# Kernel tuning notes

Measured on AMD Instinct MI355X. Metric: run time of the kernel, lower is better.

Reference implementation:

```python
import jax, jax.numpy as jnp
import numpy as np

N_NODES = 20000
N_EDGES = 640000
B = 256
GNN_DIM = 256
HID = 512
INNER = 2048
RANK = 512
N_CLASSES = 3
N_GENES = 6640


def _ln(x, s, b, eps=1e-5):
    mu = jnp.mean(x, axis=-1, keepdims=True)
    var = jnp.mean(jnp.square(x - mu), axis=-1, keepdims=True)
    return (x - mu) * jax.lax.rsqrt(var + eps) * s + b


def setup_inputs() -> dict:
    key = jax.random.key(0)
    ks = jax.random.split(key, 16)
    s = 0.02
    return {
        "node_indices": jax.random.randint(ks[0], (B,), 0, N_NODES, dtype=jnp.int32),
        "edge_index": jax.random.randint(ks[1], (2, N_EDGES), 0, N_NODES, dtype=jnp.int32),
        "edge_weight": jax.random.uniform(ks[2], (N_EDGES,), dtype=jnp.float32),
        "partial_emb": jax.random.normal(ks[3], (N_NODES, GNN_DIM), dtype=jnp.float32),
        "oov_emb": jnp.zeros((1, GNN_DIM), jnp.float32),
        "gnn_ln_s": jnp.ones((3, GNN_DIM), jnp.float32),
        "gnn_ln_b": jnp.zeros((3, GNN_DIM), jnp.float32),
        "gnn_w": jax.random.normal(ks[4], (3, GNN_DIM, GNN_DIM), jnp.float32) * s,
        "gnn_b": jnp.zeros((3, GNN_DIM), jnp.float32),
        "post_w": jax.random.normal(ks[5], (GNN_DIM, GNN_DIM), jnp.float32) * s,
        "post_b": jnp.zeros((GNN_DIM,), jnp.float32),
        "pin_w": jax.random.normal(ks[6], (GNN_DIM, HID), jnp.float32) * s,
        "pin_b": jnp.zeros((HID,), jnp.float32),
        "blk_ln_s": jnp.ones((6, HID), jnp.float32),
        "blk_ln_b": jnp.zeros((6, HID), jnp.float32),
        "blk_w1": jax.random.normal(ks[7], (6, HID, INNER), jnp.float32) * s,
        "blk_b1": jnp.zeros((6, INNER), jnp.float32),
        "blk_w2": jax.random.normal(ks[8], (6, INNER, HID), jnp.float32) * s,
        "blk_b2": jnp.zeros((6, HID), jnp.float32),
        "pout_w": jax.random.normal(ks[9], (HID, N_CLASSES * RANK), jnp.float32) * s,
        "pout_b": jnp.zeros((N_CLASSES * RANK,), jnp.float32),
        "out_gene_emb": jax.random.normal(ks[10], (N_GENES, RANK), jnp.float32) * s,
    }


def reference(node_indices, edge_index, edge_weight, partial_emb, oov_emb,
              gnn_ln_s, gnn_ln_b, gnn_w, gnn_b, post_w, post_b,
              pin_w, pin_b, blk_ln_s, blk_ln_b, blk_w1, blk_b1, blk_w2, blk_b2,
              pout_w, pout_b, out_gene_emb):
    n = partial_emb.shape[0]
    src, dst = edge_index[0], edge_index[1]
    # --- trainable GNN tail: 3 layers of (LN -> weighted scatter-sum -> Linear -> ReLU) + residual ---
    x = partial_emb
    for i in range(3):
        h = _ln(x, gnn_ln_s[i], gnn_ln_b[i])
        msg = h[src] * edge_weight[:, None]              # [E, 256] gather (memory-bound)
        agg = jax.ops.segment_sum(msg, dst, num_segments=n)
        h = jax.nn.relu(agg @ gnn_w[i] + gnn_b[i])
        x = h + x
    x = x @ post_w + post_b                              # post_mp
    # --- OOV-safe perturbation embedding lookup ---
    oov = node_indices < 0
    safe = jnp.where(oov, 0, node_indices)
    pert = jnp.where(oov[:, None], oov_emb, x[safe])     # [B, 256]
    # --- bilinear head ---
    h = pert @ pin_w + pin_b
    for i in range(6):
        z = _ln(h, blk_ln_s[i], blk_ln_b[i])
        z = jax.nn.gelu(z @ blk_w1[i] + blk_b1[i], approximate=False)
        h = h + z @ blk_w2[i] + blk_b2[i]                # dropout = identity (eval)
    proj = (h @ pout_w + pout_b).reshape(h.shape[0], N_CLASSES, RANK)
    logits = jnp.einsum('bcr,gr->bcg', proj, out_gene_emb)
    return logits
```

## Files before the change

### kernel.cpp

```cpp
#include <hip/hip_runtime.h>
#include <hip/hip_bf16.h>
#include <math.h>

#define NNODES 20000
#define NEDGES 640000
#define BSZ 256
#define GDIM 256
#define HID 512
#define INNER 2048
#define RANK 512
#define NCLS 3
#define NGENES 6640

typedef __attribute__((ext_vector_type(8))) short bf16x8;
typedef __attribute__((ext_vector_type(4))) float f32x4;
typedef __attribute__((ext_vector_type(4))) unsigned u32x4;

__device__ inline float bf2f(unsigned short u) {
    return __uint_as_float(((unsigned)u) << 16);
}
__device__ inline unsigned short f2bf(float f) {
    unsigned u = __float_as_uint(f);
    u = u + 0x7fff + ((u >> 16) & 1);
    return (unsigned short)(u >> 16);
}
__device__ inline unsigned pk2(float a, float b) {
    return (unsigned)f2bf(a) | ((unsigned)f2bf(b) << 16);
}

__device__ inline u32x4 ld16_cg(const void* p) {
    u32x4 r;
    asm volatile("global_load_dwordx4 %0, %1, off sc0 sc1" : "=v"(r) : "v"(p) : "memory");
    return r;
}
__device__ inline void st4f_cg(void* p, float v) {
    asm volatile("global_store_dword %0, %1, off sc0 sc1" :: "v"(p), "v"(v) : "memory");
}
__device__ inline void st2_cg(void* p, unsigned short v) {
    unsigned w = v;
    asm volatile("global_store_short %0, %1, off sc0 sc1" :: "v"(p), "v"(w) : "memory");
}
__device__ inline void waitvm0(void) {
    asm volatile("s_waitcnt vmcnt(0)" ::: "memory");
    __builtin_amdgcn_sched_barrier(0);
}

__global__ void hist_k(const int* __restrict__ dst, int* __restrict__ counts, int E) {
    int e = blockIdx.x * 256 + threadIdx.x;
    if (e < E) atomicAdd(&counts[dst[e]], 1);
}

__global__ void scan1_k(const int* __restrict__ counts, int* __restrict__ incl,
                        int* __restrict__ bsums, int n) {
    __shared__ int s[256];
    int i = blockIdx.x * 256 + threadIdx.x;
    int v = (i < n) ? counts[i] : 0;
    s[threadIdx.x] = v;
    __syncthreads();
    for (int off = 1; off < 256; off <<= 1) {
        int t = (threadIdx.x >= off) ? s[threadIdx.x - off] : 0;
        __syncthreads();
        s[threadIdx.x] += t;
        __syncthreads();
    }
    if (i < n) incl[i] = s[threadIdx.x];
    if (threadIdx.x == 255) bsums[blockIdx.x] = s[255];
}

__global__ void scan2_k(const int* __restrict__ bsums, int* __restrict__ boffs, int nb) {
    __shared__ int s[128];
    int tid = threadIdx.x;
    int v = (tid < nb) ? bsums[tid] : 0;
    s[tid] = v;
    __syncthreads();
    for (int off = 1; off < 128; off <<= 1) {
        int t = (tid >= off) ? s[tid - off] : 0;
        __syncthreads();
        s[tid] += t;
        __syncthreads();
    }
    if (tid < nb) boffs[tid] = s[tid] - v;
}

__global__ void scan3_k(const int* __restrict__ incl, const int* __restrict__ counts,
                        const int* __restrict__ boffs, int* __restrict__ row_start,
                        int* __restrict__ cursor, int n) {
    int i = blockIdx.x * 256 + threadIdx.x;
    if (i < n) {
        int st = incl[i] - counts[i] + boffs[blockIdx.x];
        row_start[i] = st;
        cursor[i] = st;
    }
}

__global__ void scatter_k(const int* __restrict__ src, const int* __restrict__ dst,
                          const float* __restrict__ w, int* __restrict__ cursor,
                          int2* __restrict__ ep, int E) {
    int e = blockIdx.x * 256 + threadIdx.x;
    if (e < E) {
        int d = dst[e];
        int p = atomicAdd(&cursor[d], 1);
        ep[p] = make_int2(src[e], __float_as_int(w[e]));
    }
}

__global__ void convall_k(const float* __restrict__ gnn_w, const float* __restrict__ post_w,
                          const float* __restrict__ pin_w, const float* __restrict__ blk_w1,
                          const float* __restrict__ blk_w2, const float* __restrict__ pout_w,
                          const float* __restrict__ gene, unsigned short* __restrict__ gnnT,
                          unsigned short* __restrict__ postT, unsigned short* __restrict__ pinT,
                          unsigned short* __restrict__ w1T, unsigned short* __restrict__ w2T,
                          unsigned short* __restrict__ poutT,
                          unsigned short* __restrict__ geneb) {
    int b = blockIdx.x;
    if (b >= 13440) {
        int t = b - 13440;
        const float4* xp = (const float4*)gene;
        int i = t * 512 + threadIdx.x * 2;
        float4 a = xp[i], c = xp[i + 1];
        *(ushort4*)(geneb + (size_t)i * 4) =
            make_ushort4(f2bf(a.x), f2bf(a.y), f2bf(a.z), f2bf(a.w));
        *(ushort4*)(geneb + (size_t)i * 4 + 4) =
            make_ushort4(f2bf(c.x), f2bf(c.y), f2bf(c.z), f2bf(c.w));
        return;
    }
    const float* W;
    unsigned short* WT;
    int K, N, tile;
    if (b < 192) {
        int l = b >> 6;
        tile = b & 63;
        W = gnn_w + (size_t)l * GDIM * GDIM;
        WT = gnnT + (size_t)l * GDIM * GDIM;
        K = GDIM; N = GDIM;
    } else if (b < 256) {
        tile = b - 192; W = post_w; WT = postT; K = GDIM; N = GDIM;
    } else if (b < 384) {
        tile = b - 256; W = pin_w; WT = pinT; K = GDIM; N = HID;
    } else if (b < 6528) {
        int t = b - 384;
        int l = t >> 10;
        tile = t & 1023;
        W = blk_w1 + (size_t)l * HID * INNER;
        WT = w1T + (size_t)l * INNER * HID;
        K = HID; N = INNER;
    } else if (b < 12672) {
        int t = b - 6528;
        int l = t >> 10;
        tile = t & 1023;
        W = blk_w2 + (size_t)l * INNER * HID;
        WT = w2T + (size_t)l * HID * INNER;
        K = INNER; N = HID;
    } else {
        tile = b - 12672; W = pout_w; WT = poutT; K = HID; N = NCLS * RANK;
    }
    __shared__ float s[32][33];
    int ntx = N >> 5;
    int k0 = (tile / ntx) << 5;
    int n0 = (tile % ntx) << 5;
    int tx = threadIdx.x & 31, ty = threadIdx.x >> 5;
#pragma unroll
    for (int i = 0; i < 4; i++)
        s[ty + 8 * i][tx] = W[(size_t)(k0 + ty + 8 * i) * N + n0 + tx];
    __syncthreads();
#pragma unroll
    for (int i = 0; i < 4; i++)
        WT[(size_t)(n0 + ty + 8 * i) * K + k0 + tx] = f2bf(s[tx][ty + 8 * i]);
}

__global__ void lnb_k(const float* __restrict__ X, const float* __restrict__ sc,
                      const float* __restrict__ bi, unsigned short* __restrict__ Y, int M) {
    int row = blockIdx.x * 4 + (threadIdx.x >> 6);
    int lane = threadIdx.x & 63;
    if (row >= M) return;
    float4 v = ((const float4*)(X + (size_t)row * GDIM))[lane];
    float sum = v.x + v.y + v.z + v.w;
#pragma unroll
    for (int off = 32; off >= 1; off >>= 1) sum += __shfl_xor(sum, off);
    float mu = sum / GDIM;
    float a = v.x - mu, b = v.y - mu, c = v.z - mu, d = v.w - mu;
    float sq = a * a + b * b + c * c + d * d;
#pragma unroll
    for (int off = 32; off >= 1; off >>= 1) sq += __shfl_xor(sq, off);
    float rstd = rsqrtf(sq / GDIM + 1e-5f);
    float4 s4 = ((const float4*)sc)[lane];
    float4 b4 = ((const float4*)bi)[lane];
    *(ushort4*)(Y + (size_t)row * GDIM + lane * 4) =
        make_ushort4(f2bf(a * rstd * s4.x + b4.x), f2bf(b * rstd * s4.y + b4.y),
                     f2bf(c * rstd * s4.z + b4.z), f2bf(d * rstd * s4.w + b4.w));
}

__device__ inline void agg_row(int beg, int cnt, int lane, const int2* __restrict__ ep,
                               const unsigned short* __restrict__ H, float& a0, float& a1,
                               float& a2, float& a3) {
    int t = 0;
    for (; t + 16 <= cnt; t += 16) {
        int2 e[16];
#pragma unroll
        for (int u = 0; u < 16; u++) e[u] = ep[beg + t + u];
        ushort4 v[16];
#pragma unroll
        for (int u = 0; u < 16; u++)
            v[u] = *(const ushort4*)(H + (size_t)e[u].x * GDIM + lane * 4);
#pragma unroll
        for (int u = 0; u < 16; u++) {
            float w = __int_as_float(e[u].y);
            a0 = fmaf(bf2f(v[u].x), w, a0);
            a1 = fmaf(bf2f(v[u].y), w, a1);
            a2 = fmaf(bf2f(v[u].z), w, a2);
            a3 = fmaf(bf2f(v[u].w), w, a3);
        }
    }
    for (; t + 4 <= cnt; t += 4) {
        int2 e[4];
#pragma unroll
        for (int u = 0; u < 4; u++) e[u] = ep[beg + t + u];
        ushort4 v[4];
#pragma unroll
        for (int u = 0; u < 4; u++)
            v[u] = *(const ushort4*)(H + (size_t)e[u].x * GDIM + lane * 4);
#pragma unroll
        for (int u = 0; u < 4; u++) {
            float w = __int_as_float(e[u].y);
            a0 = fmaf(bf2f(v[u].x), w, a0);
            a1 = fmaf(bf2f(v[u].y), w, a1);
            a2 = fmaf(bf2f(v[u].z), w, a2);
            a3 = fmaf(bf2f(v[u].w), w, a3);
        }
    }
    for (; t < cnt; t++) {
        int2 e = ep[beg + t];
        float w = __int_as_float(e.y);
        ushort4 v = *(const ushort4*)(H + (size_t)e.x * GDIM + lane * 4);
        a0 = fmaf(bf2f(v.x), w, a0);
        a1 = fmaf(bf2f(v.y), w, a1);
        a2 = fmaf(bf2f(v.z), w, a2);
        a3 = fmaf(bf2f(v.w), w, a3);
    }
}

__global__ void aggb_k(const int* __restrict__ row_start, const int* __restrict__ counts,
                       const int2* __restrict__ ep, const unsigned short* __restrict__ H,
                       unsigned short* __restrict__ AGG, int n) {
    int row = blockIdx.x * 4 + (threadIdx.x >> 6);
    int lane = threadIdx.x & 63;
    if (row >= n) return;
    float a0 = 0.f, a1 = 0.f, a2 = 0.f, a3 = 0.f;
    agg_row(row_start[row], counts[row], lane, ep, H, a0, a1, a2, a3);
    *(ushort4*)(AGG + (size_t)row * GDIM + lane * 4) =
        make_ushort4(f2bf(a0), f2bf(a1), f2bf(a2), f2bf(a3));
}

__global__ void aggsel_k(const int* __restrict__ idx, const int* __restrict__ row_start,
                         const int* __restrict__ counts, const int2* __restrict__ ep,
                         const unsigned short* __restrict__ H, unsigned short* __restrict__ AGG) {
    int b = blockIdx.x * 4 + (threadIdx.x >> 6);
    int lane = threadIdx.x & 63;
    int id = idx[b];
    int row = id < 0 ? 0 : id;
    float a0 = 0.f, a1 = 0.f, a2 = 0.f, a3 = 0.f;
    agg_row(row_start[row], counts[row], lane, ep, H, a0, a1, a2, a3);
    *(ushort4*)(AGG + (size_t)b * GDIM + lane * 4) =
        make_ushort4(f2bf(a0), f2bf(a1), f2bf(a2), f2bf(a3));
}

template <int ACT, bool RES, bool BIAS>
__global__ __launch_bounds__(256) void mgemm_k(const unsigned short* __restrict__ A,
                                               const unsigned short* __restrict__ BT,
                                               const float* __restrict__ bias,
                                               const float* __restrict__ R,
                                               float* __restrict__ C, int M, int N, int K) {
    __shared__ unsigned short As[128 * 32];
    __shared__ unsigned short Bs[128 * 32];
    int m0 = blockIdx.y * 128, n0 = blockIdx.x * 128;
    int tid = threadIdx.x;
    int wave = tid >> 6, lane = tid & 63;
    int wm = (wave >> 1) * 64, wn = (wave & 1) * 64;
    int lrow = lane & 15, lq = lane >> 4;

    f32x4 acc[4][4];
    const f32x4 zz = {0.f, 0.f, 0.f, 0.f};
#pragma unroll
    for (int i = 0; i < 4; i++)
#pragma unroll
        for (int j = 0; j < 4; j++) acc[i][j] = zz;

    int r0 = tid >> 2;
    int q = tid & 3;

    for (int k0 = 0; k0 < K; k0 += 32) {
#pragma unroll
        for (int p = 0; p < 2; p++) {
            int row = r0 + p * 64;
            int gm = m0 + row;
            uint4 va = make_uint4(0, 0, 0, 0);
            if (gm < M) va = *(const uint4*)(A + (size_t)gm * K + k0 + q * 8);
            *(uint4*)&As[row * 32 + q * 8] = va;
            int gn = n0 + row;
            uint4 vb = make_uint4(0, 0, 0, 0);
            if (gn < N) vb = *(const uint4*)(BT + (size_t)gn * K + k0 + q * 8);
            *(uint4*)&Bs[row * 32 + q * 8] = vb;
        }
        __syncthreads();
        bf16x8 af[4], bf[4];
#pragma unroll
        for (int i = 0; i < 4; i++)
            af[i] = *(const bf16x8*)&As[(wm + i * 16 + lrow) * 32 + lq * 8];
#pragma unroll
        for (int j = 0; j < 4; j++)
            bf[j] = *(const bf16x8*)&Bs[(wn + j * 16 + lrow) * 32 + lq * 8];
#pragma unroll
        for (int i = 0; i < 4; i++)
#pragma unroll
            for (int j = 0; j < 4; j++)
                acc[i][j] =
                    __builtin_amdgcn_mfma_f32_16x16x32_bf16(af[i], bf[j], acc[i][j], 0, 0, 0);
        __syncthreads();
    }

#pragma unroll
    for (int i = 0; i < 4; i++) {
#pragma unroll
        for (int j = 0; j < 4; j++) {
            int gn = n0 + wn + j * 16 + lrow;
            if (gn >= N) continue;
            float bv = BIAS ? bias[gn] : 0.f;
#pragma unroll
            for (int r = 0; r < 4; r++) {
                int gm = m0 + wm + i * 16 + lq * 4 + r;
                if (gm >= M) continue;
                float v = acc[i][j][r] + bv;
                if (ACT == 1) v = fmaxf(v, 0.f);
                if (RES) v += R[(size_t)gm * N + gn];
                C[(size_t)gm * N + gn] = v;
            }
        }
    }
}

template <int ACT, int EPI>
__global__ __launch_bounds__(256) void mfull_k(const unsigned short* __restrict__ A,
                                               const unsigned short* __restrict__ BT,
                                               const float* __restrict__ bias,
                                               const int* __restrict__ idx,
                                               const float* __restrict__ aux,
                                               unsigned short* __restrict__ O, int M, int N,
                                               int K) {
    __shared__ unsigned short As[64 * 32];
    __shared__ unsigned short Bs[64 * 32];
    int m0 = blockIdx.y * 64, n0 = blockIdx.x * 64;
    int tid = threadIdx.x;
    int wave = tid >> 6, lane = tid & 63;
    int wm = wave * 16;
    int lrow = lane & 15, lq = lane >> 4;
    f32x4 acc[4];
    const f32x4 zz = {0.f, 0.f, 0.f, 0.f};
#pragma unroll
    for (int j = 0; j < 4; j++) acc[j] = zz;
    int r0 = tid >> 2;
    int q = tid & 3;
    for (int k0 = 0; k0 < K; k0 += 32) {
        *(uint4*)&As[r0 * 32 + q * 8] = *(const uint4*)(A + (size_t)(m0 + r0) * K + k0 + q * 8);
        *(uint4*)&Bs[r0 * 32 + q * 8] = *(const uint4*)(BT + (size_t)(n0 + r0) * K + k0 + q * 8);
        __syncthreads();
        bf16x8 af = *(const bf16x8*)&As[(wm + lrow) * 32 + lq * 8];
#pragma unroll
        for (int j = 0; j < 4; j++) {
            bf16x8 bfr = *(const bf16x8*)&Bs[(j * 16 + lrow) * 32 + lq * 8];
            acc[j] = __builtin_amdgcn_mfma_f32_16x16x32_bf16(af, bfr, acc[j], 0, 0, 0);
        }
        __syncthreads();
    }
#pragma unroll
    for (int j = 0; j < 4; j++) {
        int gn = n0 + j * 16 + lrow;
        float bv = bias[gn];
#pragma unroll
        for (int r = 0; r < 4; r++) {
            int gm = m0 + wm + lq * 4 + r;
            float v = acc[j][r] + bv;
            if (ACT == 1) v = fmaxf(v, 0.f);
            if (ACT == 2) v = 0.5f * v * (1.f + erff(v * 0.70710678118654752f));
            if (EPI == 2) {
                int id = idx[gm];
                int safe = id < 0 ? 0 : id;
                v += aux[(size_t)safe * N + gn];
            }
            if (EPI == 1) {
                if (idx[gm] < 0) v = aux[gn];
            }
            O[(size_t)gm * N + gn] = f2bf(v);
        }
    }
}


#define HGRID 256
#define LDPA 520
#define GBLK 32

__device__ inline void gsync(int* bar, int target) {
    waitvm0();
    __syncthreads();
    if (threadIdx.x == 0) {
        __hip_atomic_fetch_add(bar, 1, __ATOMIC_RELAXED, __HIP_MEMORY_SCOPE_AGENT);
        while (__hip_atomic_load(bar, __ATOMIC_RELAXED, __HIP_MEMORY_SCOPE_AGENT) < target)
            __builtin_amdgcn_s_sleep(2);
    }
    __syncthreads();
}

template <int ROWS, int KC, bool CG>
__device__ inline void stage_issue(const unsigned short* src, int ld, u32x4* regs) {
    constexpr int NL = ROWS * KC / 8 / 256;
    int tid = threadIdx.x;
#pragma unroll
    for (int it = 0; it < NL; it++) {
        int unit = it * 256 + tid;
        int row = unit / (KC / 8);
        int ucol = unit % (KC / 8);
        const unsigned short* p = src + (size_t)row * ld + ucol * 8;
        if (CG) regs[it] = ld16_cg(p);
        else regs[it] = *(const u32x4*)p;
    }
}
template <int ROWS, int KC>
__device__ inline void stage_write(unsigned short* dst, const u32x4* regs) {
    constexpr int NL = ROWS * KC / 8 / 256;
    int tid = threadIdx.x;
#pragma unroll
    for (int it = 0; it < NL; it++) {
        int unit = it * 256 + tid;
        int row = unit / (KC / 8);
        int ucol = unit % (KC / 8);
        *(u32x4*)&dst[row * LDPA + ucol * 8] = regs[it];
    }
}

template <int KC>
__device__ inline void mma_all(const unsigned short* As, const unsigned short* Bs, f32x4 acc[2]) {
    int tid = threadIdx.x, wave = tid >> 6, lane = tid & 63;
    int wm = (wave >> 1) * 16, wn = (wave & 1) * 32;
    int lrow = lane & 15, lq = lane >> 4;
#pragma unroll
    for (int kk = 0; kk < KC / 32; kk++) {
        bf16x8 af = *(const bf16x8*)&As[(wm + lrow) * LDPA + kk * 32 + lq * 8];
#pragma unroll
        for (int j = 0; j < 2; j++) {
            bf16x8 bfr = *(const bf16x8*)&Bs[(wn + j * 16 + lrow) * LDPA + kk * 32 + lq * 8];
            acc[j] = __builtin_amdgcn_mfma_f32_16x16x32_bf16(af, bfr, acc[j], 0, 0, 0);
        }
    }
}

__global__ __launch_bounds__(256) void head_k(
    const unsigned short* __restrict__ pertbf, const unsigned short* __restrict__ pinT,
    const float* __restrict__ pin_b, const float* __restrict__ blk_ln_s,
    const float* __restrict__ blk_ln_b, const unsigned short* __restrict__ w1T,
    const float* __restrict__ blk_b1, const unsigned short* __restrict__ w2T,
    const float* __restrict__ blk_b2, const unsigned short* __restrict__ poutT,
    const float* __restrict__ pout_b, float* __restrict__ hbuf,
    unsigned short* __restrict__ z1bf, unsigned short* __restrict__ projb,
    int* __restrict__ bar) {
    __shared__ unsigned short As[32 * LDPA];
    __shared__ unsigned short Bs[64 * LDPA];
    int b = blockIdx.x;
    int g = b >> 5;
    int t = b & 31;
    int* gbar = bar + g * 32;
    int m0 = g * 32;
    int tid = threadIdx.x;
    int wave = tid >> 6, lane = tid & 63;
    int wm = (wave >> 1) * 16, wn = (wave & 1) * 32;
    int lrow = lane & 15, lq = lane >> 4;
    int ph = 0;
    f32x4 acc[2];
    const f32x4 zz = {0.f, 0.f, 0.f, 0.f};

    if (t < 8) {
        int n0 = t * 64;
        u32x4 wreg[8], areg[4];
        stage_issue<64, 256, false>(pinT + (size_t)n0 * GDIM, GDIM, wreg);
        stage_issue<32, 256, false>(pertbf + (size_t)m0 * GDIM, GDIM, areg);
        waitvm0();
        stage_write<64, 256>(Bs, wreg);
        stage_write<32, 256>(As, areg);
        __syncthreads();
        acc[0] = zz; acc[1] = zz;
        mma_all<256>(As, Bs, acc);
#pragma unroll
        for (int j = 0; j < 2; j++) {
            int gn = n0 + wn + j * 16 + lrow;
            float bv = pin_b[gn];
#pragma unroll
            for (int r = 0; r < 4; r++) {
                int gm = m0 + wm + lq * 4 + r;
                st4f_cg(hbuf + (size_t)gm * HID + gn, acc[j][r] + bv);
            }
        }
    }
    gsync(gbar, ++ph * GBLK);

    for (int i = 0; i < 6; i++) {
        {
            int n0 = t * 64;
            u32x4 wreg[16], hreg[16];
            stage_issue<64, 512, false>(w1T + (size_t)i * INNER * HID + (size_t)n0 * HID, HID,
                                        wreg);
#pragma unroll
            for (int rr = 0; rr < 8; rr++) {
                const float* p = hbuf + (size_t)(m0 + wave * 8 + rr) * HID + lane * 8;
                hreg[2 * rr] = ld16_cg(p);
                hreg[2 * rr + 1] = ld16_cg(p + 4);
            }
            waitvm0();
            stage_write<64, 512>(Bs, wreg);
            const float* ls = blk_ln_s + (size_t)i * HID;
            const float* lb = blk_ln_b + (size_t)i * HID;
            float4 s0 = ((const float4*)ls)[lane * 2], s1 = ((const float4*)ls)[lane * 2 + 1];
            float4 t0 = ((const float4*)lb)[lane * 2], t1 = ((const float4*)lb)[lane * 2 + 1];
#pragma unroll
            for (int rr = 0; rr < 8; rr++) {
                float f0 = __uint_as_float(hreg[2 * rr][0]);
                float f1 = __uint_as_float(hreg[2 * rr][1]);
                float f2 = __uint_as_float(hreg[2 * rr][2]);
                float f3 = __uint_as_float(hreg[2 * rr][3]);
                float f4 = __uint_as_float(hreg[2 * rr + 1][0]);
                float f5 = __uint_as_float(hreg[2 * rr + 1][1]);
                float f6 = __uint_as_float(hreg[2 * rr + 1][2]);
                float f7 = __uint_as_float(hreg[2 * rr + 1][3]);
                float sum = f0 + f1 + f2 + f3 + f4 + f5 + f6 + f7;
#pragma unroll
                for (int off = 32; off >= 1; off >>= 1) sum += __shfl_xor(sum, off);
                float mu = sum * (1.f / HID);
                float d0 = f0 - mu, d1 = f1 - mu, d2 = f2 - mu, d3 = f3 - mu;
                float d4 = f4 - mu, d5 = f5 - mu, d6 = f6 - mu, d7 = f7 - mu;
                float sq = d0 * d0 + d1 * d1 + d2 * d2 + d3 * d3 + d4 * d4 + d5 * d5 +
                           d6 * d6 + d7 * d7;
#pragma unroll
                for (int off = 32; off >= 1; off >>= 1) sq += __shfl_xor(sq, off);
                float rstd = rsqrtf(sq * (1.f / HID) + 1e-5f);
                u32x4 pk;
                pk[0] = pk2(d0 * rstd * s0.x + t0.x, d1 * rstd * s0.y + t0.y);
                pk[1] = pk2(d2 * rstd * s0.z + t0.z, d3 * rstd * s0.w + t0.w);
                pk[2] = pk2(d4 * rstd * s1.x + t1.x, d5 * rstd * s1.y + t1.y);
                pk[3] = pk2(d6 * rstd * s1.z + t1.z, d7 * rstd * s1.w + t1.w);
                *(u32x4*)&As[(wave * 8 + rr) * LDPA + lane * 8] = pk;
            }
            __syncthreads();
            acc[0] = zz; acc[1] = zz;
            mma_all<512>(As, Bs, acc);
#pragma unroll
            for (int j = 0; j < 2; j++) {
                int gn = n0 + wn + j * 16 + lrow;
                float bv = blk_b1[(size_t)i * INNER + gn];
#pragma unroll
                for (int r = 0; r < 4; r++) {
                    int gm = m0 + wm + lq * 4 + r;
                    float v = acc[j][r] + bv;
                    v = 0.5f * v * (1.f + erff(v * 0.70710678118654752f));
                    st2_cg(z1bf + (size_t)gm * INNER + gn, f2bf(v));
                }
            }
        }
        gsync(gbar, ++ph * GBLK);
        {
            int s = t >> 3, n0 = (t & 7) * 64, kbeg = s * 512;
            u32x4 wreg[16], areg[8];
            stage_issue<64, 512, false>(
                w2T + (size_t)i * HID * INNER + (size_t)n0 * INNER + kbeg, INNER, wreg);
            stage_issue<32, 512, true>(z1bf + (size_t)m0 * INNER + kbeg, INNER, areg);
            waitvm0();
            stage_write<64, 512>(Bs, wreg);
            stage_write<32, 512>(As, areg);
            __syncthreads();
            acc[0] = zz; acc[1] = zz;
            mma_all<512>(As, Bs, acc);
#pragma unroll
            for (int j = 0; j < 2; j++) {
                int gn = n0 + wn + j * 16 + lrow;
                float bv = (s == 0) ? blk_b2[(size_t)i * HID + gn] : 0.f;
#pragma unroll
                for (int r = 0; r < 4; r++) {
                    int gm = m0 + wm + lq * 4 + r;
                    __hip_atomic_fetch_add(hbuf + (size_t)gm * HID + gn, acc[j][r] + bv,
                                           __ATOMIC_RELAXED, __HIP_MEMORY_SCOPE_AGENT);
                }
            }
        }
        gsync(gbar, ++ph * GBLK);
    }

    if (t < 24) {
        int n0 = t * 64;
        u32x4 wreg[16], areg[16];
        stage_issue<64, 512, false>(poutT + (size_t)n0 * HID, HID, wreg);
#pragma unroll
        for (int it = 0; it < 16; it++) {
            int unit = it * 256 + tid;
            int row = unit >> 7, ucol = unit & 127;
            areg[it] = ld16_cg(hbuf + (size_t)(m0 + row) * HID + ucol * 4);
        }
        waitvm0();
        stage_write<64, 512>(Bs, wreg);
#pragma unroll
        for (int it = 0; it < 16; it++) {
            int unit = it * 256 + tid;
            int row = unit >> 7, ucol = unit & 127;
            float a = __uint_as_float(areg[it][0]), c = __uint_as_float(areg[it][1]);
            float d = __uint_as_float(areg[it][2]), e = __uint_as_float(areg[it][3]);
            uint2 w2v;
            w2v.x = pk2(a, c);
            w2v.y = pk2(d, e);
            *(uint2*)&As[row * LDPA + ucol * 4] = w2v;
        }
        __syncthreads();
        acc[0] = zz; acc[1] = zz;
        mma_all<512>(As, Bs, acc);
#pragma unroll
        for (int j = 0; j < 2; j++) {
            int gn = n0 + wn + j * 16 + lrow;
            float bv = pout_b[gn];
#pragma unroll
            for (int r = 0; r < 4; r++) {
                int gm = m0 + wm + lq * 4 + r;
                projb[(size_t)gm * (NCLS * RANK) + gn] = f2bf(acc[j][r] + bv);
            }
        }
    }
}

extern "C" void kernel_launch(void* const* d_in, const int* in_sizes, int n_in,
                              void* d_out, int out_size, void* d_ws, size_t ws_size,
                              hipStream_t stream) {
    const int* node_indices = (const int*)d_in[0];
    const int* edge_src = (const int*)d_in[1];
    const int* edge_dst = edge_src + NEDGES;
    const float* edge_w = (const float*)d_in[2];
    const float* partial_emb = (const float*)d_in[3];
    const float* oov_emb = (const float*)d_in[4];
    const float* gnn_ln_s = (const float*)d_in[5];
    const float* gnn_ln_b = (const float*)d_in[6];
    const float* gnn_w = (const float*)d_in[7];
    const float* gnn_b = (const float*)d_in[8];
    const float* post_w = (const float*)d_in[9];
    const float* post_b = (const float*)d_in[10];
    const float* pin_w = (const float*)d_in[11];
    const float* pin_b = (const float*)d_in[12];
    const float* blk_ln_s = (const float*)d_in[13];
    const float* blk_ln_b = (const float*)d_in[14];
    const float* blk_w1 = (const float*)d_in[15];
    const float* blk_b1 = (const float*)d_in[16];
    const float* blk_w2 = (const float*)d_in[17];
    const float* blk_b2 = (const float*)d_in[18];
    const float* pout_w = (const float*)d_in[19];
    const float* pout_b = (const float*)d_in[20];
    const float* gene = (const float*)d_in[21];
    float* out = (float*)d_out;

    char* p = (char*)d_ws;
    auto alloc = [&](size_t bytes) {
        char* r = p;
        p += (bytes + 255) & ~(size_t)255;
        return r;
    };
    int* counts = (int*)alloc(NNODES * 4);
    int* incl = (int*)alloc(NNODES * 4);
    int* bsums = (int*)alloc(128 * 4);
    int* boffs = (int*)alloc(128 * 4);
    int* row_start = (int*)alloc(NNODES * 4);
    int* cursor = (int*)alloc(NNODES * 4);
    int2* epack = (int2*)alloc((size_t)NEDGES * 8);
    float* part = (float*)alloc((size_t)NNODES * GDIM * 4);
    unsigned short* ln_bf = (unsigned short*)part;
    unsigned short* aggbf = (unsigned short*)((char*)part + (size_t)NNODES * GDIM * 2);
    float* xa = (float*)alloc((size_t)NNODES * GDIM * 4);
    float* xb = (float*)alloc((size_t)NNODES * GDIM * 4);
    float* hbuf = (float*)alloc((size_t)BSZ * HID * 4);
    unsigned short* aggselb = (unsigned short*)alloc((size_t)BSZ * GDIM * 2);
    unsigned short* pertinbf = (unsigned short*)alloc((size_t)BSZ * GDIM * 2);
    unsigned short* pertbf = (unsigned short*)alloc((size_t)BSZ * GDIM * 2);
    unsigned short* zlnbf = (unsigned short*)alloc((size_t)BSZ * HID * 2);
    unsigned short* z1bf = (unsigned short*)alloc((size_t)BSZ * INNER * 2);
    unsigned short* hbufbf = (unsigned short*)alloc((size_t)BSZ * HID * 2);
    unsigned short* projb = (unsigned short*)alloc((size_t)BSZ * NCLS * RANK * 2);
    unsigned short* gnnT = (unsigned short*)alloc((size_t)3 * GDIM * GDIM * 2);
    unsigned short* postT = (unsigned short*)alloc((size_t)GDIM * GDIM * 2);
    unsigned short* pinT = (unsigned short*)alloc((size_t)HID * GDIM * 2);
    unsigned short* w1T = (unsigned short*)alloc((size_t)6 * INNER * HID * 2);
    unsigned short* w2T = (unsigned short*)alloc((size_t)6 * HID * INNER * 2);
    unsigned short* poutT = (unsigned short*)alloc((size_t)NCLS * RANK * HID * 2);
    unsigned short* geneb = (unsigned short*)alloc((size_t)NGENES * RANK * 2);
    int* bar = (int*)alloc(1024);

    const int EB = (NEDGES + 255) / 256;
    const int NB = (NNODES + 255) / 256;

    convall_k<<<15100, 256, 0, stream>>>(gnn_w, post_w, pin_w, blk_w1, blk_w2, pout_w, gene,
                                         gnnT, postT, pinT, w1T, w2T, poutT, geneb);

    (void)hipMemsetAsync(counts, 0, NNODES * 4, stream);
    (void)hipMemsetAsync(bar, 0, 1024, stream);
    hist_k<<<EB, 256, 0, stream>>>(edge_dst, counts, NEDGES);
    scan1_k<<<NB, 256, 0, stream>>>(counts, incl, bsums, NNODES);
    scan2_k<<<1, 128, 0, stream>>>(bsums, boffs, NB);
    scan3_k<<<NB, 256, 0, stream>>>(incl, counts, boffs, row_start, cursor, NNODES);
    scatter_k<<<EB, 256, 0, stream>>>(edge_src, edge_dst, edge_w, cursor, epack, NEDGES);

    const float* x_in = partial_emb;
    float* bufs[2] = {xa, xb};
    for (int i = 0; i < 2; i++) {
        lnb_k<<<(NNODES + 3) / 4, 256, 0, stream>>>(x_in, gnn_ln_s + i * GDIM,
                                                    gnn_ln_b + i * GDIM, ln_bf, NNODES);
        aggb_k<<<(NNODES + 3) / 4, 256, 0, stream>>>(row_start, counts, epack, ln_bf, aggbf,
                                                     NNODES);
        float* x_out = bufs[i];
        mgemm_k<1, true, true><<<dim3(GDIM / 128, (NNODES + 127) / 128), 256, 0, stream>>>(
            aggbf, gnnT + (size_t)i * GDIM * GDIM, gnn_b + i * GDIM, x_in, x_out, NNODES, GDIM,
            GDIM);
        x_in = x_out;
    }
    lnb_k<<<(NNODES + 3) / 4, 256, 0, stream>>>(xb, gnn_ln_s + 2 * GDIM, gnn_ln_b + 2 * GDIM,
                                                ln_bf, NNODES);
    aggsel_k<<<BSZ / 4, 256, 0, stream>>>(node_indices, row_start, counts, epack, ln_bf, aggselb);
    mfull_k<1, 2><<<dim3(GDIM / 64, BSZ / 64), 256, 0, stream>>>(
        aggselb, gnnT + (size_t)2 * GDIM * GDIM, gnn_b + 2 * GDIM, node_indices, xb, pertinbf,
        BSZ, GDIM, GDIM);

    mfull_k<0, 1><<<dim3(GDIM / 64, BSZ / 64), 256, 0, stream>>>(
        pertinbf, postT, post_b, node_indices, oov_emb, pertbf, BSZ, GDIM, GDIM);

    head_k<<<HGRID, 256, 0, stream>>>(pertbf, pinT, pin_b, blk_ln_s, blk_ln_b, w1T, blk_b1, w2T,
                                      blk_b2, poutT, pout_b, hbuf, z1bf, projb, bar);

    mgemm_k<0, false, false><<<dim3((NGENES + 127) / 128, (BSZ * NCLS) / 128), 256, 0, stream>>>(
        projb, geneb, nullptr, nullptr, out, BSZ * NCLS, NGENES, RANK);
}
```

Baseline: 555.2 us.

## Restrict layer-2 aggregation to needed nodes and prefetch head weights across barriers

Adds a flag kernel that marks the queried nodes and their in-neighbours, so the second-layer aggregation and the final LayerNorm only process rows whose values reach the output. This removes most of the gather work in layer 2 and most of the last LN pass, at the cost of an extra memset and a small flag kernel. In the head kernel, the next stage's weight tile is issued into a register buffer before each grid barrier, so the weight loads overlap the synchronisation wait, at the cost of more live registers. The layer-2 GEMM still runs on every row, including rows whose aggregation input is now stale but never used.

```diff
diff --git a/kernel.cpp b/kernel.cpp
--- a/kernel.cpp
+++ b/kernel.cpp
@@ -102,6 +102,18 @@
         int p = atomicAdd(&cursor[d], 1);
         ep[p] = make_int2(src[e], __float_as_int(w[e]));
     }
+}
+
+__global__ void flag_k(const int* __restrict__ idx, const int* __restrict__ row_start,
+                       const int* __restrict__ counts, const int2* __restrict__ ep,
+                       int* __restrict__ flag) {
+    int r4 = blockIdx.x * 4 + (threadIdx.x >> 6);
+    int lane = threadIdx.x & 63;
+    int id = idx[r4];
+    int row = id < 0 ? 0 : id;
+    if (lane == 0) flag[row] = 1;
+    int beg = row_start[row], cnt = counts[row];
+    for (int t = lane; t < cnt; t += 64) flag[ep[beg + t].x] = 1;
 }
 
 __global__ void convall_k(const float* __restrict__ gnn_w, const float* __restrict__ post_w,
@@ -168,11 +180,14 @@
         WT[(size_t)(n0 + ty + 8 * i) * K + k0 + tx] = f2bf(s[tx][ty + 8 * i]);
 }
 
+template <bool FLAGGED>
 __global__ void lnb_k(const float* __restrict__ X, const float* __restrict__ sc,
-                      const float* __restrict__ bi, unsigned short* __restrict__ Y, int M) {
+                      const float* __restrict__ bi, unsigned short* __restrict__ Y, int M,
+                      const int* __restrict__ flag) {
     int row = blockIdx.x * 4 + (threadIdx.x >> 6);
     int lane = threadIdx.x & 63;
     if (row >= M) return;
+    if (FLAGGED && !flag[row]) return;
     float4 v = ((const float4*)(X + (size_t)row * GDIM))[lane];
     float sum = v.x + v.y + v.z + v.w;
 #pragma unroll
@@ -239,12 +254,14 @@
     }
 }
 
+template <bool FLAGGED>
 __global__ void aggb_k(const int* __restrict__ row_start, const int* __restrict__ counts,
                        const int2* __restrict__ ep, const unsigned short* __restrict__ H,
-                       unsigned short* __restrict__ AGG, int n) {
+                       unsigned short* __restrict__ AGG, int n, const int* __restrict__ flag) {
     int row = blockIdx.x * 4 + (threadIdx.x >> 6);
     int lane = threadIdx.x & 63;
     if (row >= n) return;
+    if (FLAGGED && !flag[row]) return;
     float a0 = 0.f, a1 = 0.f, a2 = 0.f, a3 = 0.f;
     agg_row(row_start[row], counts[row], lane, ep, H, a0, a1, a2, a3);
     *(ushort4*)(AGG + (size_t)row * GDIM + lane * 4) =
@@ -476,6 +493,7 @@
     int ph = 0;
     f32x4 acc[2];
     const f32x4 zz = {0.f, 0.f, 0.f, 0.f};
+    u32x4 pf[16];
 
     if (t < 8) {
         int n0 = t * 64;
@@ -499,22 +517,21 @@
             }
         }
     }
+    stage_issue<64, 512, false>(w1T + (size_t)t * 64 * HID, HID, pf);
     gsync(gbar, ++ph * GBLK);
 
     for (int i = 0; i < 6; i++) {
         {
             int n0 = t * 64;
-            u32x4 wreg[16], hreg[16];
-            stage_issue<64, 512, false>(w1T + (size_t)i * INNER * HID + (size_t)n0 * HID, HID,
-                                        wreg);
+            u32x4 hreg[16];
 #pragma unroll
             for (int rr = 0; rr < 8; rr++) {
                 const float* p = hbuf + (size_t)(m0 + wave * 8 + rr) * HID + lane * 8;
                 hreg[2 * rr] = ld16_cg(p);
                 hreg[2 * rr + 1] = ld16_cg(p + 4);
             }
+            stage_write<64, 512>(Bs, pf);
             waitvm0();
-            stage_write<64, 512>(Bs, wreg);
             const float* ls = blk_ln_s + (size_t)i * HID;
             const float* lb = blk_ln_b + (size_t)i * HID;
             float4 s0 = ((const float4*)ls)[lane * 2], s1 = ((const float4*)ls)[lane * 2 + 1];
@@ -562,16 +579,17 @@
                     st2_cg(z1bf + (size_t)gm * INNER + gn, f2bf(v));
                 }
             }
+            stage_issue<64, 512, false>(
+                w2T + (size_t)i * HID * INNER + (size_t)(t & 7) * 64 * INNER + (t >> 3) * 512,
+                INNER, pf);
         }
         gsync(gbar, ++ph * GBLK);
         {
             int s = t >> 3, n0 = (t & 7) * 64, kbeg = s * 512;
-            u32x4 wreg[16], areg[8];
-            stage_issue<64, 512, false>(
-                w2T + (size_t)i * HID * INNER + (size_t)n0 * INNER + kbeg, INNER, wreg);
+            u32x4 areg[8];
             stage_issue<32, 512, true>(z1bf + (size_t)m0 * INNER + kbeg, INNER, areg);
+            stage_write<64, 512>(Bs, pf);
             waitvm0();
-            stage_write<64, 512>(Bs, wreg);
             stage_write<32, 512>(As, areg);
             __syncthreads();
             acc[0] = zz; acc[1] = zz;
@@ -587,22 +605,26 @@
                                            __ATOMIC_RELAXED, __HIP_MEMORY_SCOPE_AGENT);
                 }
             }
+            if (i < 5)
+                stage_issue<64, 512, false>(
+                    w1T + (size_t)(i + 1) * INNER * HID + (size_t)t * 64 * HID, HID, pf);
+            else if (t < 24)
+                stage_issue<64, 512, false>(poutT + (size_t)t * 64 * HID, HID, pf);
         }
         gsync(gbar, ++ph * GBLK);
     }
 
     if (t < 24) {
         int n0 = t * 64;
-        u32x4 wreg[16], areg[16];
-        stage_issue<64, 512, false>(poutT + (size_t)n0 * HID, HID, wreg);
+        u32x4 areg[16];
 #pragma unroll
         for (int it = 0; it < 16; it++) {
             int unit = it * 256 + tid;
             int row = unit >> 7, ucol = unit & 127;
             areg[it] = ld16_cg(hbuf + (size_t)(m0 + row) * HID + ucol * 4);
         }
+        stage_write<64, 512>(Bs, pf);
         waitvm0();
-        stage_write<64, 512>(Bs, wreg);
 #pragma unroll
         for (int it = 0; it < 16; it++) {
             int unit = it * 256 + tid;
@@ -670,6 +692,7 @@
     int* boffs = (int*)alloc(128 * 4);
     int* row_start = (int*)alloc(NNODES * 4);
     int* cursor = (int*)alloc(NNODES * 4);
+    int* flag = (int*)alloc(NNODES * 4);
     int2* epack = (int2*)alloc((size_t)NEDGES * 8);
     float* part = (float*)alloc((size_t)NNODES * GDIM * 4);
     unsigned short* ln_bf = (unsigned short*)part;
@@ -680,9 +703,7 @@
     unsigned short* aggselb = (unsigned short*)alloc((size_t)BSZ * GDIM * 2);
     unsigned short* pertinbf = (unsigned short*)alloc((size_t)BSZ * GDIM * 2);
     unsigned short* pertbf = (unsigned short*)alloc((size_t)BSZ * GDIM * 2);
-    unsigned short* zlnbf = (unsigned short*)alloc((size_t)BSZ * HID * 2);
     unsigned short* z1bf = (unsigned short*)alloc((size_t)BSZ * INNER * 2);
-    unsigned short* hbufbf = (unsigned short*)alloc((size_t)BSZ * HID * 2);
     unsigned short* projb = (unsigned short*)alloc((size_t)BSZ * NCLS * RANK * 2);
     unsigned short* gnnT = (unsigned short*)alloc((size_t)3 * GDIM * GDIM * 2);
     unsigned short* postT = (unsigned short*)alloc((size_t)GDIM * GDIM * 2);
@@ -700,28 +721,34 @@
                                          gnnT, postT, pinT, w1T, w2T, poutT, geneb);
 
     (void)hipMemsetAsync(counts, 0, NNODES * 4, stream);
+    (void)hipMemsetAsync(flag, 0, NNODES * 4, stream);
     (void)hipMemsetAsync(bar, 0, 1024, stream);
     hist_k<<<EB, 256, 0, stream>>>(edge_dst, counts, NEDGES);
     scan1_k<<<NB, 256, 0, stream>>>(counts, incl, bsums, NNODES);
     scan2_k<<<1, 128, 0, stream>>>(bsums, boffs, NB);
     scan3_k<<<NB, 256, 0, stream>>>(incl, counts, boffs, row_start, cursor, NNODES);
     scatter_k<<<EB, 256, 0, stream>>>(edge_src, edge_dst, edge_w, cursor, epack, NEDGES);
+    flag_k<<<BSZ / 4, 256, 0, stream>>>(node_indices, row_start, counts, epack, flag);
 
     const float* x_in = partial_emb;
     float* bufs[2] = {xa, xb};
     for (int i = 0; i < 2; i++) {
-        lnb_k<<<(NNODES + 3) / 4, 256, 0, stream>>>(x_in, gnn_ln_s + i * GDIM,
-                                                    gnn_ln_b + i * GDIM, ln_bf, NNODES);
-        aggb_k<<<(NNODES + 3) / 4, 256, 0, stream>>>(row_start, counts, epack, ln_bf, aggbf,
-                                                     NNODES);
+        lnb_k<false><<<(NNODES + 3) / 4, 256, 0, stream>>>(
+            x_in, gnn_ln_s + i * GDIM, gnn_ln_b + i * GDIM, ln_bf, NNODES, nullptr);
+        if (i == 0)
+            aggb_k<false><<<(NNODES + 3) / 4, 256, 0, stream>>>(row_start, counts, epack, ln_bf,
+                                                                aggbf, NNODES, nullptr);
+        else
+            aggb_k<true><<<(NNODES + 3) / 4, 256, 0, stream>>>(row_start, counts, epack, ln_bf,
+                                                               aggbf, NNODES, flag);
         float* x_out = bufs[i];
         mgemm_k<1, true, true><<<dim3(GDIM / 128, (NNODES + 127) / 128), 256, 0, stream>>>(
             aggbf, gnnT + (size_t)i * GDIM * GDIM, gnn_b + i * GDIM, x_in, x_out, NNODES, GDIM,
             GDIM);
         x_in = x_out;
     }
-    lnb_k<<<(NNODES + 3) / 4, 256, 0, stream>>>(xb, gnn_ln_s + 2 * GDIM, gnn_ln_b + 2 * GDIM,
-                                                ln_bf, NNODES);
+    lnb_k<true><<<(NNODES + 3) / 4, 256, 0, stream>>>(xb, gnn_ln_s + 2 * GDIM,
+                                                      gnn_ln_b + 2 * GDIM, ln_bf, NNODES, flag);
     aggsel_k<<<BSZ / 4, 256, 0, stream>>>(node_indices, row_start, counts, epack, ln_bf, aggselb);
     mfull_k<1, 2><<<dim3(GDIM / 64, BSZ / 64), 256, 0, stream>>>(
         aggselb, gnnT + (size_t)2 * GDIM * GDIM, gnn_b + 2 * GDIM, node_indices, xb, pertinbf,
```

New measurement: 526.6 us. 5.1% less time.
